# Kernel tuning notes

Measured on AMD Instinct MI355X. Metric: run time of the kernel, lower is better.

## Reference

```python
import jax, jax.numpy as jnp
import numpy as np

H = 1024      # hidden_dim
NH = 16       # num_heads
HD = H // NH  # head_dim
EPS = 1e-12
SCALE = float(np.sqrt(H))


def setup_inputs() -> dict:
    key = jax.random.key(0)
    ks = jax.random.split(key, 12)
    S, B = 2048, 2
    inp = {
        "query": jax.random.normal(ks[0], (S, B, 2 * H), jnp.float32),
        "key":   jax.random.normal(ks[1], (S, B, H), jnp.float32),
        "value": jax.random.normal(ks[2], (S, B, H), jnp.float32),
        # gating params (zeros in torch init, but randomize for a meaningful test)
        "qs": jax.random.normal(ks[3], (1, 1, H), jnp.float32) * 0.02,
        "ks_p": jax.random.normal(ks[4], (1, 1, H), jnp.float32) * 0.02,
        "vs": jax.random.normal(ks[5], (1, 1, H), jnp.float32) * 0.02,
        # Overparam vq: Linear(H, 2H)
        "vq_w": jax.random.normal(ks[6], (2 * H, H), jnp.float32) * (1.0 / np.sqrt(H)),
        "vq_b": jax.random.normal(ks[7], (2 * H,), jnp.float32) * 0.02,
        # q_linear: Linear(2H, H)
        "ql_w": jax.random.normal(ks[8], (H, 2 * H), jnp.float32) * (1.0 / np.sqrt(2 * H)),
        "ql_b": jax.random.normal(ks[9], (H,), jnp.float32) * 0.02,
        # LayerNorm(H)
        "ln_g": jnp.ones((H,), jnp.float32),
        "ln_b": jnp.zeros((H,), jnp.float32),
    }
    return inp


def _layernorm(x, g, b):
    mu = jnp.mean(x, axis=-1, keepdims=True)
    var = jnp.mean(jnp.square(x - mu), axis=-1, keepdims=True)
    return (x - mu) * jax.lax.rsqrt(var + EPS) * g + b


def reference(query, key, value, qs, ks_p, vs, vq_w, vq_b, ql_w, ql_b, ln_g, ln_b):
    # gate vectors
    qsig = jax.nn.sigmoid(qs)            # [1,1,H]
    ksig = jax.nn.sigmoid(ks_p)          # [1,1,H]
    # vq = Overparam(sigmoid(vs)): c,f = l1(x).split(H); sigmoid(f)*tanh(c)
    h = jax.nn.sigmoid(vs) @ vq_w.T + vq_b   # [1,1,2H]
    c, f = h[..., :H], h[..., H:]
    vsig = jax.nn.sigmoid(f) * jnp.tanh(c)   # [1,1,H]

    q = qsig * _layernorm(query @ ql_w.T + ql_b, ln_g, ln_b)  # [S,B,H]
    k = ksig * key
    v = vsig * value

    # batch-first
    q = jnp.transpose(q, (1, 0, 2))  # [B,Q,H]
    k = jnp.transpose(k, (1, 0, 2))  # [B,K,H]
    v = jnp.transpose(v, (1, 0, 2))
    B, Q, _ = q.shape
    K = k.shape[1]

    qh = q.reshape(B, Q, NH, HD)
    kh = k.reshape(B, K, NH, HD)
    vh = v.reshape(B, K, NH, HD)

    scores = jnp.einsum('bqhd,bkhd->bhqk', qh, kh) / SCALE
    w = jax.nn.softmax(scores, axis=-1)                # [B,NH,Q,K]
    out = jnp.einsum('bhqk,bkhd->bqhd', w, vh).reshape(B, Q, H)
    # torch code's final .transpose(0,1) is not assigned -> output is [Q,B,H]
    return jnp.transpose(out, (1, 0, 2))
```

## Files before the change

kernel.cpp:

```cpp
#include <hip/hip_runtime.h>

typedef __bf16 bf16x8 __attribute__((ext_vector_type(8)));
typedef float f32x4 __attribute__((ext_vector_type(4)));
typedef unsigned short u16x8 __attribute__((ext_vector_type(8)));
typedef unsigned short u16x4 __attribute__((ext_vector_type(4)));
typedef unsigned short u16;
typedef unsigned int u32;


#define LOG2E 1.4426950408889634f

__device__ __forceinline__ float b2f(u16 u) {
  union { unsigned int i; float f; } x; x.i = ((unsigned int)u) << 16; return x.f;
}
__device__ __forceinline__ u16 f2b(float f) {
  union { float f; unsigned int i; } x; x.f = f;
  unsigned int r = (x.i + 0x7fffu + ((x.i >> 16) & 1u)) >> 16;
  return (u16)r;
}
__device__ __forceinline__ float sigm(float x) { return 1.0f / (1.0f + __expf(-x)); }
__device__ __forceinline__ u32 cvtpk(float lo, float hi) {
  u32 r; asm("v_cvt_pk_bf16_f32 %0, %1, %2" : "=v"(r) : "v"(lo), "v"(hi)); return r;
}

__device__ __forceinline__ void async16(u16* lds, const u16* g) {
  __builtin_amdgcn_global_load_lds((const __attribute__((address_space(1))) void*)g,
                                   (__attribute__((address_space(3))) void*)lds, 16, 0, 0);
}

__global__ __launch_bounds__(256) void k_cvt_h(const float4* __restrict__ q, u16x4* __restrict__ qd,
                                               const float4* __restrict__ w, u16x4* __restrict__ wd,
                                               const float4* __restrict__ k, u16x4* __restrict__ kd,
                                               const float4* __restrict__ v, u16x4* __restrict__ vd,
                                               const float* __restrict__ vs,
                                               const float* __restrict__ vq_w,
                                               const float* __restrict__ vq_b,
                                               float* __restrict__ h,
                                               const float* __restrict__ qs,
                                               const float* __restrict__ ks,
                                               float* __restrict__ gate) {
  __shared__ float svs[1024];
  int b = blockIdx.x;
  int t = threadIdx.x;
  if (b < 2048) {
#pragma unroll
    for (int vb = b; vb < 18432; vb += 2048) {
      const float4* s; u16x4* d; int i;
      if (vb < 8192)       { s = q; d = qd; i = vb * 256 + t; }
      else if (vb < 10240) { s = w; d = wd; i = (vb - 8192) * 256 + t; }
      else if (vb < 14336) { s = k; d = kd; i = (vb - 10240) * 256 + t; }
      else                 { s = v; d = vd; i = (vb - 14336) * 256 + t; }
      float4 x = s[i];
      u16x4 o; o[0] = f2b(x.x); o[1] = f2b(x.y); o[2] = f2b(x.z); o[3] = f2b(x.w);
      d[i] = o;
    }
    return;
  }
  if (b < 2560) {
    for (int i = t; i < 1024; i += 256) svs[i] = sigm(vs[i]);
    __syncthreads();
    int wave = t >> 6, lane = t & 63;
    int row = (b - 2048) * 4 + wave;
    const float4* w4 = (const float4*)(vq_w + (size_t)row * 1024);
    const float4* s4 = (const float4*)svs;
    float acc = 0.f;
#pragma unroll
    for (int kk = 0; kk < 4; ++kk) {
      float4 wv = w4[kk * 64 + lane];
      float4 sv = s4[kk * 64 + lane];
      acc += wv.x * sv.x + wv.y * sv.y + wv.z * sv.z + wv.w * sv.w;
    }
#pragma unroll
    for (int off = 1; off < 64; off <<= 1) acc += __shfl_xor(acc, off);
    if (lane == 0) h[row] = acc + vq_b[row];
    return;
  }
  int ch = (b - 2560) * 256 + t;
  gate[ch] = sigm(qs[ch]) * sigm(ks[ch]) * (LOG2E / 32.0f);
}

__global__ __launch_bounds__(256) void k_gemm(const u16* __restrict__ A,
                                              const u16* __restrict__ Bt,
                                              u16* __restrict__ C) {
  __shared__ __align__(16) u16 As[2][64 * 32];
  __shared__ __align__(16) u16 Bs[2][128 * 32];
  int tid = threadIdx.x;
  int wave = tid >> 6, lane = tid & 63;
  int l15 = lane & 15, quad = lane >> 4;
  int bx = blockIdx.x & 511;
  int kh = blockIdx.x >> 9;
  int kofs = kh << 10;
  int m0 = (bx >> 3) * 64;
  int n0 = (bx & 7) * 128;
  int wm = (wave >> 1) * 32, wn = (wave & 1) * 64;
  f32x4 acc[2][4] = {};
  int c1 = tid, c2 = tid + 256;
  const u16* gaA = A + (size_t)(m0 + (c1 >> 2)) * 2048 + kofs + (c1 & 3) * 8;
  const u16* gb1 = Bt + (size_t)(n0 + (c1 >> 2)) * 2048 + kofs + (c1 & 3) * 8;
  const u16* gb2 = Bt + (size_t)(n0 + (c2 >> 2)) * 2048 + kofs + (c2 & 3) * 8;
  int lofs = wave * 512;
  async16(As[0] + lofs, gaA);
  async16(Bs[0] + lofs, gb1); async16(Bs[0] + 2048 + lofs, gb2);
  gaA += 32; gb1 += 32; gb2 += 32;
  __syncthreads();
  for (int kt = 0; kt < 32; ++kt) {
    int cur = kt & 1;
    if (kt < 31) {
      async16(As[cur ^ 1] + lofs, gaA);
      async16(Bs[cur ^ 1] + lofs, gb1); async16(Bs[cur ^ 1] + 2048 + lofs, gb2);
      gaA += 32; gb1 += 32; gb2 += 32;
    }
    bf16x8 af[2], bfr[4];
#pragma unroll
    for (int mt = 0; mt < 2; ++mt)
      af[mt] = *(const bf16x8*)(As[cur] + (wm + mt * 16 + l15) * 32 + quad * 8);
#pragma unroll
    for (int nt = 0; nt < 4; ++nt)
      bfr[nt] = *(const bf16x8*)(Bs[cur] + (wn + nt * 16 + l15) * 32 + quad * 8);
#pragma unroll
    for (int mt = 0; mt < 2; ++mt)
#pragma unroll
      for (int nt = 0; nt < 4; ++nt)
        acc[mt][nt] = __builtin_amdgcn_mfma_f32_16x16x32_bf16(af[mt], bfr[nt], acc[mt][nt], 0, 0, 0);
    __syncthreads();
  }
  u16* Cp = C + (size_t)kh * 4096 * 1024;
#pragma unroll
  for (int mt = 0; mt < 2; ++mt) {
#pragma unroll
    for (int r = 0; r < 4; ++r) {
      int m = m0 + wm + mt * 16 + quad * 4 + r;
      u16* crow = Cp + (size_t)m * 1024 + n0 + wn + l15;
#pragma unroll
      for (int nt = 0; nt < 4; ++nt) crow[nt * 16] = f2b(acc[mt][nt][r]);
    }
  }
}

__global__ __launch_bounds__(256) void k_ln(const u16* __restrict__ qpre0,
                                            const u16* __restrict__ qpre1,
                                            const float* __restrict__ ql_b,
                                            const float* __restrict__ ln_g,
                                            const float* __restrict__ ln_b,
                                            const float* __restrict__ gate,
                                            u16* __restrict__ qatt) {
  int t = threadIdx.x;
  int wave = t >> 6, lane = t & 63;
  int row = blockIdx.x * 4 + wave;
  int ch0 = lane * 16;
  const u16* p0 = qpre0 + (size_t)row * 1024 + ch0;
  const u16* p1 = qpre1 + (size_t)row * 1024 + ch0;
  u16x8 a0 = *(const u16x8*)p0;
  u16x8 a1 = *(const u16x8*)(p0 + 8);
  u16x8 c0 = *(const u16x8*)p1;
  u16x8 c1 = *(const u16x8*)(p1 + 8);
  float qb[16];
#pragma unroll
  for (int i = 0; i < 4; ++i) *(float4*)&qb[i * 4] = *(const float4*)(ql_b + ch0 + i * 4);
  float v[16];
  float s = 0.f, ss = 0.f;
#pragma unroll
  for (int j = 0; j < 8; ++j) {
    v[j] = b2f(a0[j]) + b2f(c0[j]) + qb[j];
    v[8 + j] = b2f(a1[j]) + b2f(c1[j]) + qb[8 + j];
  }
#pragma unroll
  for (int j = 0; j < 16; ++j) { s += v[j]; ss += v[j] * v[j]; }
#pragma unroll
  for (int off = 1; off < 64; off <<= 1) { s += __shfl_xor(s, off); ss += __shfl_xor(ss, off); }
  float mu = s * (1.f / 1024.f);
  float rstd = rsqrtf(ss * (1.f / 1024.f) - mu * mu + 1e-12f);
  float g_[16], bb[16], gt[16];
#pragma unroll
  for (int i = 0; i < 4; ++i) {
    *(float4*)&g_[i * 4] = *(const float4*)(ln_g + ch0 + i * 4);
    *(float4*)&bb[i * 4] = *(const float4*)(ln_b + ch0 + i * 4);
    *(float4*)&gt[i * 4] = *(const float4*)(gate + ch0 + i * 4);
  }
  int sidx = row >> 1, b = row & 1;
  int hh = ch0 >> 6, hd0 = ch0 & 63;
  u16* dst = qatt + ((size_t)(b * 16 + hh) * 2048 + sidx) * 64 + hd0;
  u16x8 o0, o1;
#pragma unroll
  for (int j = 0; j < 8; ++j) {
    o0[j] = f2b(((v[j] - mu) * rstd * g_[j] + bb[j]) * gt[j]);
    o1[j] = f2b(((v[8 + j] - mu) * rstd * g_[8 + j] + bb[8 + j]) * gt[8 + j]);
  }
  *(u16x8*)dst = o0;
  *(u16x8*)(dst + 8) = o1;
}

__device__ __forceinline__ f32x4 mfma16(bf16x8 a, bf16x8 b, f32x4 c) {
  return __builtin_amdgcn_mfma_f32_16x16x32_bf16(a, b, c, 0, 0, 0);
}

template <int CUR>
__device__ __forceinline__ void attn_iter(bool pref,
                                          const bf16x8 (&qf)[4][2],
                                          const u16*& kp, const u16*& vp,
                                          u16 (&Ks)[2][64 * 64], u16 (&Vt)[2][64 * 64],
                                          f32x4 (&oacc)[4][4], float (&l_i)[4],
                                          int kdst, int chbase, int pcol,
                                          int l15, int kh, int kcolA, int kcolB, int vcol) {
  const u16* kt0 = Ks[CUR] + (kh * 32 + l15) * 64;
  bf16x8 kA0 = *(const bf16x8*)(kt0 + kcolA);
  bf16x8 kB0 = *(const bf16x8*)(kt0 + kcolB);
  bf16x8 kA1 = *(const bf16x8*)(kt0 + 16 * 64 + kcolA);
  bf16x8 kB1 = *(const bf16x8*)(kt0 + 16 * 64 + kcolB);
  f32x4 sacc[4][2] = {};
  __builtin_amdgcn_s_setprio(1);
#pragma unroll
  for (int f = 0; f < 4; ++f) {
    sacc[f][0] = mfma16(kA0, qf[f][0], sacc[f][0]);
    sacc[f][0] = mfma16(kB0, qf[f][1], sacc[f][0]);
    sacc[f][1] = mfma16(kA1, qf[f][0], sacc[f][1]);
    sacc[f][1] = mfma16(kB1, qf[f][1], sacc[f][1]);
  }
  __builtin_amdgcn_s_setprio(0);
  u16x8 kr0, kr1, va, vq;
  if (pref) {
    kp += 64 * 2048;
    kr0 = *(const u16x8*)kp;
    kr1 = *(const u16x8*)(kp + (size_t)32 * 2048);
    vp += 64 * 2048;
    va = *(const u16x8*)vp;
    vq = *(const u16x8*)(vp + 2048);
  }
  union U8 { u32 w[4]; bf16x8 v; };
  bf16x8 pa[4];
#pragma unroll
  for (int f = 0; f < 4; ++f) {
    float pe[2][4];
#pragma unroll
    for (int kn = 0; kn < 2; ++kn)
#pragma unroll
      for (int r = 0; r < 4; ++r) pe[kn][r] = __builtin_amdgcn_exp2f(sacc[f][kn][r]);
    l_i[f] += (pe[0][0] + pe[0][1] + pe[0][2] + pe[0][3]) +
              (pe[1][0] + pe[1][1] + pe[1][2] + pe[1][3]);
    U8 t;
    t.w[0] = cvtpk(pe[0][0], pe[0][1]); t.w[1] = cvtpk(pe[0][2], pe[0][3]);
    t.w[2] = cvtpk(pe[1][0], pe[1][1]); t.w[3] = cvtpk(pe[1][2], pe[1][3]);
    pa[f] = t.v;
  }
  const u16* vt0 = Vt[CUR];
  __builtin_amdgcn_s_setprio(1);
#pragma unroll
  for (int nt = 0; nt < 4; ++nt) {
    bf16x8 vF = *(const bf16x8*)(vt0 + (nt * 16 + l15) * 64 + vcol);
    oacc[0][nt] = mfma16(pa[0], vF, oacc[0][nt]);
    oacc[1][nt] = mfma16(pa[1], vF, oacc[1][nt]);
    oacc[2][nt] = mfma16(pa[2], vF, oacc[2][nt]);
    oacc[3][nt] = mfma16(pa[3], vF, oacc[3][nt]);
  }
  __builtin_amdgcn_s_setprio(0);
  if (pref) {
    u16* kd = (u16*)Ks[CUR ^ 1];
    *(u16x8*)(kd + kdst) = kr0;
    *(u16x8*)(kd + kdst + 2048) = kr1;
    u16* vd = (u16*)Vt[CUR ^ 1];
#pragma unroll
    for (int c = 0; c < 8; ++c) {
      u32 pk2 = (u32)va[c] | ((u32)vq[c] << 16);
      *(u32*)&vd[(chbase + c) * 64 + (pcol ^ (c << 3))] = pk2;
    }
  }
  __syncthreads();
}

__device__ __forceinline__ void donate2(float* Rw, float* Lxp,
                                        const f32x4 (&o0)[4], const f32x4 (&o1)[4],
                                        float l0, float l1, int quad, int l15) {
#pragma unroll
  for (int nt = 0; nt < 4; ++nt)
#pragma unroll
    for (int r = 0; r < 4; ++r) {
      Rw[(quad * 4 + r) * 64 + nt * 16 + l15] = o0[nt][r];
      Rw[(16 + quad * 4 + r) * 64 + nt * 16 + l15] = o1[nt][r];
    }
  if (quad == 0) { Lxp[l15] = l0; Lxp[16 + l15] = l1; }
}

__device__ __forceinline__ void epi2(const float* Rr, const float* Lxp,
                                     const f32x4 (&o0)[4], const f32x4 (&o1)[4],
                                     float l0, float l1, const float (&vsg)[4],
                                     float* __restrict__ out, int sqbase, int b, int h,
                                     int quad, int l15) {
#pragma unroll
  for (int ff = 0; ff < 2; ++ff) {
    float lt = (ff == 0 ? l0 : l1) + Lxp[ff * 16 + l15];
#pragma unroll
    for (int r = 0; r < 4; ++r) {
      int sq = sqbase + ff * 16 + quad * 4 + r;
      float inv = 1.0f / __shfl(lt, quad * 4 + r);
      float* orow = out + ((size_t)sq * 2 + b) * 1024 + h * 64;
#pragma unroll
      for (int nt = 0; nt < 4; ++nt) {
        float own = (ff == 0 ? o0[nt][r] : o1[nt][r]);
        orow[nt * 16 + l15] =
            (own + Rr[(ff * 16 + quad * 4 + r) * 64 + nt * 16 + l15]) * inv * vsg[nt];
      }
    }
  }
}

__global__ __launch_bounds__(256, 2) void k_attn(const u16* __restrict__ qatt,
                                                 const u16* __restrict__ key,
                                                 const u16* __restrict__ value,
                                                 const float* __restrict__ hbuf,
                                                 float* __restrict__ out) {
  int bh = blockIdx.x & 31;
  int qt = blockIdx.x >> 5;
  int b = bh >> 4, h = bh & 15;
  int tid = threadIdx.x, wave = tid >> 6, lane = tid & 63;
  int l15 = lane & 15, quad = lane >> 4;
  int qh = wave >> 1, kh = wave & 1;
  int q0 = qt * 128;

  __shared__ __align__(16) u16 Ks[2][64 * 64];
  __shared__ __align__(16) u16 Vt[2][64 * 64];
  __shared__ float Lx[2][2][32];

  bf16x8 qf[4][2];
#pragma unroll
  for (int f = 0; f < 4; ++f) {
    const u16* qrow = qatt + ((size_t)bh * 2048 + q0 + qh * 64 + f * 16 + l15) * 64 + quad * 8;
    qf[f][0] = *(const bf16x8*)qrow;
    qf[f][1] = *(const bf16x8*)(qrow + 32);
  }

  const u16* kb = key + (size_t)b * 1024 + (size_t)h * 64;
  const u16* vb = value + (size_t)b * 1024 + (size_t)h * 64;

  int krow = tid >> 3;
  int kchk = (tid & 7) * 8;
  const u16* kp = kb + (size_t)krow * 2048 + kchk;
  int kdst = krow * 64 + (kchk ^ ((krow & 7) << 3));

  int p = lane & 31;
  int chbase = wave * 16 + (lane >> 5) * 8;
  const u16* vp = vb + (size_t)2 * p * 2048 + chbase;
  int kk = 2 * p;
  int pcol = ((kk >> 5) & 1) * 32 + ((kk >> 2) & 3) * 8 + ((kk >> 4) & 1) * 4 + (kk & 3);
  int swr = (l15 & 7) << 3;
  int kcolA = (8 * quad) ^ swr;
  int kcolB = (32 + 8 * quad) ^ swr;
  int vcol = (kh * 32 + 8 * quad) ^ swr;

  {
    u16x8 kr0 = *(const u16x8*)kp;
    u16x8 kr1 = *(const u16x8*)(kp + (size_t)32 * 2048);
    *(u16x8*)(&Ks[0][kdst]) = kr0;
    *(u16x8*)(&Ks[0][kdst + 2048]) = kr1;
    u16x8 va = *(const u16x8*)vp;
    u16x8 vq = *(const u16x8*)(vp + 2048);
#pragma unroll
    for (int c = 0; c < 8; ++c) {
      u32 pk2 = (u32)va[c] | ((u32)vq[c] << 16);
      *(u32*)&Vt[0][(chbase + c) * 64 + (pcol ^ (c << 3))] = pk2;
    }
  }
  __syncthreads();

  f32x4 oacc[4][4] = {};
  float l_i[4] = {};

  for (int kt = 0; kt < 32; kt += 2) {
    attn_iter<0>(true, qf, kp, vp, Ks, Vt, oacc, l_i, kdst, chbase, pcol, l15, kh, kcolA, kcolB, vcol);
    attn_iter<1>(kt < 30, qf, kp, vp, Ks, Vt, oacc, l_i, kdst, chbase, pcol, l15, kh, kcolA, kcolB, vcol);
  }

#pragma unroll
  for (int f = 0; f < 4; ++f) {
    float l = l_i[f];
    l += __shfl_xor(l, 16);
    l += __shfl_xor(l, 32);
    l_i[f] = l;
  }
  float* base = (qh == 0) ? (float*)&Ks[0][0] : (float*)&Vt[0][0];
  if (kh == 0) {
    donate2(base + 2048, &Lx[qh][1][0], oacc[2], oacc[3], l_i[2], l_i[3], quad, l15);
  } else {
    donate2(base, &Lx[qh][0][0], oacc[0], oacc[1], l_i[0], l_i[1], quad, l15);
  }
  __syncthreads();
  float vsg[4];
#pragma unroll
  for (int nt = 0; nt < 4; ++nt) {
    int ch = h * 64 + nt * 16 + l15;
    vsg[nt] = sigm(hbuf[1024 + ch]) * tanhf(hbuf[ch]);
  }
  int sqbase = q0 + qh * 64 + kh * 32;
  if (kh == 0) {
    epi2(base, &Lx[qh][0][0], oacc[0], oacc[1], l_i[0], l_i[1], vsg, out, sqbase, b, h, quad, l15);
  } else {
    epi2(base + 2048, &Lx[qh][1][0], oacc[2], oacc[3], l_i[2], l_i[3], vsg, out, sqbase, b, h, quad, l15);
  }
}

extern "C" void kernel_launch(void* const* d_in, const int* in_sizes, int n_in,
                              void* d_out, int out_size, void* d_ws, size_t ws_size,
                              hipStream_t stream) {
  (void)in_sizes; (void)n_in; (void)out_size; (void)ws_size;
  const float* query = (const float*)d_in[0];
  const float* key   = (const float*)d_in[1];
  const float* value = (const float*)d_in[2];
  const float* qs    = (const float*)d_in[3];
  const float* ksp   = (const float*)d_in[4];
  const float* vs    = (const float*)d_in[5];
  const float* vq_w  = (const float*)d_in[6];
  const float* vq_b  = (const float*)d_in[7];
  const float* ql_w  = (const float*)d_in[8];
  const float* ql_b  = (const float*)d_in[9];
  const float* ln_g  = (const float*)d_in[10];
  const float* ln_b  = (const float*)d_in[11];
  float* out = (float*)d_out;

  float* ws = (float*)d_ws;
  float* h    = ws;
  float* gate = ws + 2048;
  u16* qpre  = (u16*)(ws + 4096);
  u16* qbf   = qpre + (size_t)2 * 4096 * 1024;
  u16* qatt  = qbf;
  u16* wbf   = qbf + (size_t)4096 * 2048;
  u16* kbf   = wbf + (size_t)1024 * 2048;
  u16* vbf   = kbf + (size_t)4096 * 1024;

  hipLaunchKernelGGL(k_cvt_h, dim3(2564), dim3(256), 0, stream,
                     (const float4*)query, (u16x4*)qbf,
                     (const float4*)ql_w,  (u16x4*)wbf,
                     (const float4*)key,   (u16x4*)kbf,
                     (const float4*)value, (u16x4*)vbf,
                     vs, vq_w, vq_b, h, qs, ksp, gate);
  hipLaunchKernelGGL(k_gemm, dim3(1024), dim3(256), 0, stream, qbf, wbf, qpre);
  hipLaunchKernelGGL(k_ln,   dim3(1024), dim3(256), 0, stream, qpre, qpre + (size_t)4096 * 1024,
                     ql_b, ln_g, ln_b, gate, qatt);
  hipLaunchKernelGGL(k_attn, dim3(512),  dim3(256), 0, stream, qatt, kbf, vbf, h, out);
}
```

Before: 218.5 us.

## Fuse all four stages into one persistent kernel with grid barriers

Replaces the four separate launches (convert, GEMM, layernorm, attention) with a single 512-block persistent kernel that runs each stage in sequence, separated by atomic-counter grid barriers. A memset before the launch clears the barrier counters. The goal is to remove launch overhead and the gaps between kernels. In exchange, the earlier stages lose parallelism (the conversion and GEMM now use 512 blocks instead of 2564 and 1024), every stage waits on a spin barrier, and correctness depends on all 512 blocks being resident at once.

```diff
diff --git a/kernel.cpp b/kernel.cpp
--- a/kernel.cpp
+++ b/kernel.cpp
@@ -9,6 +9,7 @@
 
 
 #define LOG2E 1.4426950408889634f
+#define NBLK 512u
 
 __device__ __forceinline__ float b2f(u16 u) {
   union { unsigned int i; float f; } x; x.i = ((unsigned int)u) << 16; return x.f;
@@ -22,73 +23,33 @@
 __device__ __forceinline__ u32 cvtpk(float lo, float hi) {
   u32 r; asm("v_cvt_pk_bf16_f32 %0, %1, %2" : "=v"(r) : "v"(lo), "v"(hi)); return r;
 }
-
 __device__ __forceinline__ void async16(u16* lds, const u16* g) {
   __builtin_amdgcn_global_load_lds((const __attribute__((address_space(1))) void*)g,
                                    (__attribute__((address_space(3))) void*)lds, 16, 0, 0);
 }
-
-__global__ __launch_bounds__(256) void k_cvt_h(const float4* __restrict__ q, u16x4* __restrict__ qd,
-                                               const float4* __restrict__ w, u16x4* __restrict__ wd,
-                                               const float4* __restrict__ k, u16x4* __restrict__ kd,
-                                               const float4* __restrict__ v, u16x4* __restrict__ vd,
-                                               const float* __restrict__ vs,
-                                               const float* __restrict__ vq_w,
-                                               const float* __restrict__ vq_b,
-                                               float* __restrict__ h,
-                                               const float* __restrict__ qs,
-                                               const float* __restrict__ ks,
-                                               float* __restrict__ gate) {
-  __shared__ float svs[1024];
-  int b = blockIdx.x;
-  int t = threadIdx.x;
-  if (b < 2048) {
-#pragma unroll
-    for (int vb = b; vb < 18432; vb += 2048) {
-      const float4* s; u16x4* d; int i;
-      if (vb < 8192)       { s = q; d = qd; i = vb * 256 + t; }
-      else if (vb < 10240) { s = w; d = wd; i = (vb - 8192) * 256 + t; }
-      else if (vb < 14336) { s = k; d = kd; i = (vb - 10240) * 256 + t; }
-      else                 { s = v; d = vd; i = (vb - 14336) * 256 + t; }
-      float4 x = s[i];
-      u16x4 o; o[0] = f2b(x.x); o[1] = f2b(x.y); o[2] = f2b(x.z); o[3] = f2b(x.w);
-      d[i] = o;
-    }
-    return;
-  }
-  if (b < 2560) {
-    for (int i = t; i < 1024; i += 256) svs[i] = sigm(vs[i]);
-    __syncthreads();
-    int wave = t >> 6, lane = t & 63;
-    int row = (b - 2048) * 4 + wave;
-    const float4* w4 = (const float4*)(vq_w + (size_t)row * 1024);
-    const float4* s4 = (const float4*)svs;
-    float acc = 0.f;
-#pragma unroll
-    for (int kk = 0; kk < 4; ++kk) {
-      float4 wv = w4[kk * 64 + lane];
-      float4 sv = s4[kk * 64 + lane];
-      acc += wv.x * sv.x + wv.y * sv.y + wv.z * sv.z + wv.w * sv.w;
-    }
-#pragma unroll
-    for (int off = 1; off < 64; off <<= 1) acc += __shfl_xor(acc, off);
-    if (lane == 0) h[row] = acc + vq_b[row];
-    return;
-  }
-  int ch = (b - 2560) * 256 + t;
-  gate[ch] = sigm(qs[ch]) * sigm(ks[ch]) * (LOG2E / 32.0f);
-}
-
-__global__ __launch_bounds__(256) void k_gemm(const u16* __restrict__ A,
-                                              const u16* __restrict__ Bt,
-                                              u16* __restrict__ C) {
-  __shared__ __align__(16) u16 As[2][64 * 32];
-  __shared__ __align__(16) u16 Bs[2][128 * 32];
-  int tid = threadIdx.x;
+__device__ __forceinline__ f32x4 mfma16(bf16x8 a, bf16x8 b, f32x4 c) {
+  return __builtin_amdgcn_mfma_f32_16x16x32_bf16(a, b, c, 0, 0, 0);
+}
+
+__device__ __forceinline__ void gbar(unsigned* c) {
+  __syncthreads();
+  if (threadIdx.x == 0) {
+    __threadfence();
+    __hip_atomic_fetch_add(c, 1u, __ATOMIC_ACQ_REL, __HIP_MEMORY_SCOPE_AGENT);
+    while (__hip_atomic_load(c, __ATOMIC_ACQUIRE, __HIP_MEMORY_SCOPE_AGENT) < NBLK)
+      __builtin_amdgcn_s_sleep(2);
+    __threadfence();
+  }
+  __syncthreads();
+}
+
+__device__ __forceinline__ void gemm_tile(int bid, const u16* __restrict__ A,
+                                          const u16* __restrict__ Bt, u16* __restrict__ C,
+                                          u16* As, u16* Bs, int tid) {
   int wave = tid >> 6, lane = tid & 63;
   int l15 = lane & 15, quad = lane >> 4;
-  int bx = blockIdx.x & 511;
-  int kh = blockIdx.x >> 9;
+  int bx = bid & 511;
+  int kh = bid >> 9;
   int kofs = kh << 10;
   int m0 = (bx >> 3) * 64;
   int n0 = (bx & 7) * 128;
@@ -99,29 +60,30 @@
   const u16* gb1 = Bt + (size_t)(n0 + (c1 >> 2)) * 2048 + kofs + (c1 & 3) * 8;
   const u16* gb2 = Bt + (size_t)(n0 + (c2 >> 2)) * 2048 + kofs + (c2 & 3) * 8;
   int lofs = wave * 512;
-  async16(As[0] + lofs, gaA);
-  async16(Bs[0] + lofs, gb1); async16(Bs[0] + 2048 + lofs, gb2);
+  async16(As + lofs, gaA);
+  async16(Bs + lofs, gb1); async16(Bs + 2048 + lofs, gb2);
   gaA += 32; gb1 += 32; gb2 += 32;
   __syncthreads();
   for (int kt = 0; kt < 32; ++kt) {
     int cur = kt & 1;
     if (kt < 31) {
-      async16(As[cur ^ 1] + lofs, gaA);
-      async16(Bs[cur ^ 1] + lofs, gb1); async16(Bs[cur ^ 1] + 2048 + lofs, gb2);
+      async16(As + (cur ^ 1) * 2048 + lofs, gaA);
+      async16(Bs + (cur ^ 1) * 4096 + lofs, gb1);
+      async16(Bs + (cur ^ 1) * 4096 + 2048 + lofs, gb2);
       gaA += 32; gb1 += 32; gb2 += 32;
     }
     bf16x8 af[2], bfr[4];
 #pragma unroll
     for (int mt = 0; mt < 2; ++mt)
-      af[mt] = *(const bf16x8*)(As[cur] + (wm + mt * 16 + l15) * 32 + quad * 8);
+      af[mt] = *(const bf16x8*)(As + cur * 2048 + (wm + mt * 16 + l15) * 32 + quad * 8);
 #pragma unroll
     for (int nt = 0; nt < 4; ++nt)
-      bfr[nt] = *(const bf16x8*)(Bs[cur] + (wn + nt * 16 + l15) * 32 + quad * 8);
+      bfr[nt] = *(const bf16x8*)(Bs + cur * 4096 + (wn + nt * 16 + l15) * 32 + quad * 8);
 #pragma unroll
     for (int mt = 0; mt < 2; ++mt)
 #pragma unroll
       for (int nt = 0; nt < 4; ++nt)
-        acc[mt][nt] = __builtin_amdgcn_mfma_f32_16x16x32_bf16(af[mt], bfr[nt], acc[mt][nt], 0, 0, 0);
+        acc[mt][nt] = mfma16(af[mt], bfr[nt], acc[mt][nt]);
     __syncthreads();
   }
   u16* Cp = C + (size_t)kh * 4096 * 1024;
@@ -135,74 +97,17 @@
       for (int nt = 0; nt < 4; ++nt) crow[nt * 16] = f2b(acc[mt][nt][r]);
     }
   }
-}
-
-__global__ __launch_bounds__(256) void k_ln(const u16* __restrict__ qpre0,
-                                            const u16* __restrict__ qpre1,
-                                            const float* __restrict__ ql_b,
-                                            const float* __restrict__ ln_g,
-                                            const float* __restrict__ ln_b,
-                                            const float* __restrict__ gate,
-                                            u16* __restrict__ qatt) {
-  int t = threadIdx.x;
-  int wave = t >> 6, lane = t & 63;
-  int row = blockIdx.x * 4 + wave;
-  int ch0 = lane * 16;
-  const u16* p0 = qpre0 + (size_t)row * 1024 + ch0;
-  const u16* p1 = qpre1 + (size_t)row * 1024 + ch0;
-  u16x8 a0 = *(const u16x8*)p0;
-  u16x8 a1 = *(const u16x8*)(p0 + 8);
-  u16x8 c0 = *(const u16x8*)p1;
-  u16x8 c1 = *(const u16x8*)(p1 + 8);
-  float qb[16];
-#pragma unroll
-  for (int i = 0; i < 4; ++i) *(float4*)&qb[i * 4] = *(const float4*)(ql_b + ch0 + i * 4);
-  float v[16];
-  float s = 0.f, ss = 0.f;
-#pragma unroll
-  for (int j = 0; j < 8; ++j) {
-    v[j] = b2f(a0[j]) + b2f(c0[j]) + qb[j];
-    v[8 + j] = b2f(a1[j]) + b2f(c1[j]) + qb[8 + j];
-  }
-#pragma unroll
-  for (int j = 0; j < 16; ++j) { s += v[j]; ss += v[j] * v[j]; }
-#pragma unroll
-  for (int off = 1; off < 64; off <<= 1) { s += __shfl_xor(s, off); ss += __shfl_xor(ss, off); }
-  float mu = s * (1.f / 1024.f);
-  float rstd = rsqrtf(ss * (1.f / 1024.f) - mu * mu + 1e-12f);
-  float g_[16], bb[16], gt[16];
-#pragma unroll
-  for (int i = 0; i < 4; ++i) {
-    *(float4*)&g_[i * 4] = *(const float4*)(ln_g + ch0 + i * 4);
-    *(float4*)&bb[i * 4] = *(const float4*)(ln_b + ch0 + i * 4);
-    *(float4*)&gt[i * 4] = *(const float4*)(gate + ch0 + i * 4);
-  }
-  int sidx = row >> 1, b = row & 1;
-  int hh = ch0 >> 6, hd0 = ch0 & 63;
-  u16* dst = qatt + ((size_t)(b * 16 + hh) * 2048 + sidx) * 64 + hd0;
-  u16x8 o0, o1;
-#pragma unroll
-  for (int j = 0; j < 8; ++j) {
-    o0[j] = f2b(((v[j] - mu) * rstd * g_[j] + bb[j]) * gt[j]);
-    o1[j] = f2b(((v[8 + j] - mu) * rstd * g_[8 + j] + bb[8 + j]) * gt[8 + j]);
-  }
-  *(u16x8*)dst = o0;
-  *(u16x8*)(dst + 8) = o1;
-}
-
-__device__ __forceinline__ f32x4 mfma16(bf16x8 a, bf16x8 b, f32x4 c) {
-  return __builtin_amdgcn_mfma_f32_16x16x32_bf16(a, b, c, 0, 0, 0);
 }
 
 template <int CUR>
 __device__ __forceinline__ void attn_iter(bool pref,
                                           const bf16x8 (&qf)[4][2],
                                           const u16*& kp, const u16*& vp,
-                                          u16 (&Ks)[2][64 * 64], u16 (&Vt)[2][64 * 64],
+                                          u16* KsB, u16* VtB,
                                           f32x4 (&oacc)[4][4], float (&l_i)[4],
                                           int kdst, int chbase, int pcol,
                                           int l15, int kh, int kcolA, int kcolB, int vcol) {
-  const u16* kt0 = Ks[CUR] + (kh * 32 + l15) * 64;
+  const u16* kt0 = KsB + CUR * 4096 + (kh * 32 + l15) * 64;
   bf16x8 kA0 = *(const bf16x8*)(kt0 + kcolA);
   bf16x8 kB0 = *(const bf16x8*)(kt0 + kcolB);
   bf16x8 kA1 = *(const bf16x8*)(kt0 + 16 * 64 + kcolA);
@@ -242,7 +147,7 @@
     t.w[2] = cvtpk(pe[1][0], pe[1][1]); t.w[3] = cvtpk(pe[1][2], pe[1][3]);
     pa[f] = t.v;
   }
-  const u16* vt0 = Vt[CUR];
+  const u16* vt0 = VtB + CUR * 4096;
   __builtin_amdgcn_s_setprio(1);
 #pragma unroll
   for (int nt = 0; nt < 4; ++nt) {
@@ -254,10 +159,10 @@
   }
   __builtin_amdgcn_s_setprio(0);
   if (pref) {
-    u16* kd = (u16*)Ks[CUR ^ 1];
+    u16* kd = KsB + (CUR ^ 1) * 4096;
     *(u16x8*)(kd + kdst) = kr0;
     *(u16x8*)(kd + kdst + 2048) = kr1;
-    u16* vd = (u16*)Vt[CUR ^ 1];
+    u16* vd = VtB + (CUR ^ 1) * 4096;
 #pragma unroll
     for (int c = 0; c < 8; ++c) {
       u32 pk2 = (u32)va[c] | ((u32)vq[c] << 16);
@@ -303,97 +208,214 @@
   }
 }
 
-__global__ __launch_bounds__(256, 2) void k_attn(const u16* __restrict__ qatt,
-                                                 const u16* __restrict__ key,
-                                                 const u16* __restrict__ value,
-                                                 const float* __restrict__ hbuf,
-                                                 float* __restrict__ out) {
-  int bh = blockIdx.x & 31;
-  int qt = blockIdx.x >> 5;
-  int b = bh >> 4, h = bh & 15;
+__global__ __launch_bounds__(256, 2) void k_all(const float* __restrict__ query,
+                                                const float* __restrict__ key_,
+                                                const float* __restrict__ value,
+                                                const float* __restrict__ qs,
+                                                const float* __restrict__ ksp,
+                                                const float* __restrict__ vs,
+                                                const float* __restrict__ vq_w,
+                                                const float* __restrict__ vq_b,
+                                                const float* __restrict__ ql_w,
+                                                const float* __restrict__ ql_b,
+                                                const float* __restrict__ ln_g,
+                                                const float* __restrict__ ln_b,
+                                                float* __restrict__ out,
+                                                float* __restrict__ ws) {
+  __shared__ __align__(16) u16 SMEM[16640];
+  int blk = blockIdx.x;
   int tid = threadIdx.x, wave = tid >> 6, lane = tid & 63;
-  int l15 = lane & 15, quad = lane >> 4;
-  int qh = wave >> 1, kh = wave & 1;
-  int q0 = qt * 128;
-
-  __shared__ __align__(16) u16 Ks[2][64 * 64];
-  __shared__ __align__(16) u16 Vt[2][64 * 64];
-  __shared__ float Lx[2][2][32];
-
-  bf16x8 qf[4][2];
-#pragma unroll
-  for (int f = 0; f < 4; ++f) {
-    const u16* qrow = qatt + ((size_t)bh * 2048 + q0 + qh * 64 + f * 16 + l15) * 64 + quad * 8;
-    qf[f][0] = *(const bf16x8*)qrow;
-    qf[f][1] = *(const bf16x8*)(qrow + 32);
-  }
-
-  const u16* kb = key + (size_t)b * 1024 + (size_t)h * 64;
-  const u16* vb = value + (size_t)b * 1024 + (size_t)h * 64;
-
-  int krow = tid >> 3;
-  int kchk = (tid & 7) * 8;
-  const u16* kp = kb + (size_t)krow * 2048 + kchk;
-  int kdst = krow * 64 + (kchk ^ ((krow & 7) << 3));
-
-  int p = lane & 31;
-  int chbase = wave * 16 + (lane >> 5) * 8;
-  const u16* vp = vb + (size_t)2 * p * 2048 + chbase;
-  int kk = 2 * p;
-  int pcol = ((kk >> 5) & 1) * 32 + ((kk >> 2) & 3) * 8 + ((kk >> 4) & 1) * 4 + (kk & 3);
-  int swr = (l15 & 7) << 3;
-  int kcolA = (8 * quad) ^ swr;
-  int kcolB = (32 + 8 * quad) ^ swr;
-  int vcol = (kh * 32 + 8 * quad) ^ swr;
+
+  float* h    = ws;
+  float* gate = ws + 2048;
+  unsigned* bar = (unsigned*)(ws + 3072);
+  u16* qpre  = (u16*)(ws + 4096);
+  u16* qbf   = qpre + (size_t)2 * 4096 * 1024;
+  u16* qatt  = qbf;
+  u16* wbf   = qbf + (size_t)4096 * 2048;
+  u16* kbf   = wbf + (size_t)1024 * 2048;
+  u16* vbf   = kbf + (size_t)4096 * 1024;
 
   {
-    u16x8 kr0 = *(const u16x8*)kp;
-    u16x8 kr1 = *(const u16x8*)(kp + (size_t)32 * 2048);
-    *(u16x8*)(&Ks[0][kdst]) = kr0;
-    *(u16x8*)(&Ks[0][kdst + 2048]) = kr1;
-    u16x8 va = *(const u16x8*)vp;
-    u16x8 vq = *(const u16x8*)(vp + 2048);
-#pragma unroll
-    for (int c = 0; c < 8; ++c) {
-      u32 pk2 = (u32)va[c] | ((u32)vq[c] << 16);
-      *(u32*)&Vt[0][(chbase + c) * 64 + (pcol ^ (c << 3))] = pk2;
-    }
-  }
-  __syncthreads();
-
-  f32x4 oacc[4][4] = {};
-  float l_i[4] = {};
-
-  for (int kt = 0; kt < 32; kt += 2) {
-    attn_iter<0>(true, qf, kp, vp, Ks, Vt, oacc, l_i, kdst, chbase, pcol, l15, kh, kcolA, kcolB, vcol);
-    attn_iter<1>(kt < 30, qf, kp, vp, Ks, Vt, oacc, l_i, kdst, chbase, pcol, l15, kh, kcolA, kcolB, vcol);
-  }
-
-#pragma unroll
-  for (int f = 0; f < 4; ++f) {
-    float l = l_i[f];
-    l += __shfl_xor(l, 16);
-    l += __shfl_xor(l, 32);
-    l_i[f] = l;
-  }
-  float* base = (qh == 0) ? (float*)&Ks[0][0] : (float*)&Vt[0][0];
-  if (kh == 0) {
-    donate2(base + 2048, &Lx[qh][1][0], oacc[2], oacc[3], l_i[2], l_i[3], quad, l15);
-  } else {
-    donate2(base, &Lx[qh][0][0], oacc[0], oacc[1], l_i[0], l_i[1], quad, l15);
-  }
-  __syncthreads();
-  float vsg[4];
-#pragma unroll
-  for (int nt = 0; nt < 4; ++nt) {
-    int ch = h * 64 + nt * 16 + l15;
-    vsg[nt] = sigm(hbuf[1024 + ch]) * tanhf(hbuf[ch]);
-  }
-  int sqbase = q0 + qh * 64 + kh * 32;
-  if (kh == 0) {
-    epi2(base, &Lx[qh][0][0], oacc[0], oacc[1], l_i[0], l_i[1], vsg, out, sqbase, b, h, quad, l15);
-  } else {
-    epi2(base + 2048, &Lx[qh][1][0], oacc[2], oacc[3], l_i[2], l_i[3], vsg, out, sqbase, b, h, quad, l15);
+    const float4* q4 = (const float4*)query;
+    const float4* w4 = (const float4*)ql_w;
+    const float4* k4 = (const float4*)key_;
+    const float4* v4 = (const float4*)value;
+    for (int vb = blk; vb < 18432; vb += 512) {
+      const float4* s; u16x4* d; int i;
+      if (vb < 8192)       { s = q4; d = (u16x4*)qbf; i = vb * 256 + tid; }
+      else if (vb < 10240) { s = w4; d = (u16x4*)wbf; i = (vb - 8192) * 256 + tid; }
+      else if (vb < 14336) { s = k4; d = (u16x4*)kbf; i = (vb - 10240) * 256 + tid; }
+      else                 { s = v4; d = (u16x4*)vbf; i = (vb - 14336) * 256 + tid; }
+      float4 x = s[i];
+      u16x4 o; o[0] = f2b(x.x); o[1] = f2b(x.y); o[2] = f2b(x.z); o[3] = f2b(x.w);
+      d[i] = o;
+    }
+    float* svs = (float*)SMEM;
+    for (int i = tid; i < 1024; i += 256) svs[i] = sigm(vs[i]);
+    __syncthreads();
+    int row = blk * 4 + wave;
+    const float4* wv4 = (const float4*)(vq_w + (size_t)row * 1024);
+    const float4* s4 = (const float4*)svs;
+    float acc = 0.f;
+#pragma unroll
+    for (int kk = 0; kk < 4; ++kk) {
+      float4 wv = wv4[kk * 64 + lane];
+      float4 sv = s4[kk * 64 + lane];
+      acc += wv.x * sv.x + wv.y * sv.y + wv.z * sv.z + wv.w * sv.w;
+    }
+#pragma unroll
+    for (int off = 1; off < 64; off <<= 1) acc += __shfl_xor(acc, off);
+    if (lane == 0) h[row] = acc + vq_b[row];
+    if (tid < 2) {
+      int ch = blk * 2 + tid;
+      gate[ch] = sigm(qs[ch]) * sigm(ksp[ch]) * (LOG2E / 32.0f);
+    }
+  }
+  gbar(bar + 0);
+
+  {
+    u16* As = SMEM;
+    u16* Bs = SMEM + 4096;
+    gemm_tile(blk, qbf, wbf, qpre, As, Bs, tid);
+    gemm_tile(blk + 512, qbf, wbf, qpre, As, Bs, tid);
+  }
+  gbar(bar + 1);
+
+  {
+    const u16* qpre1 = qpre + (size_t)4096 * 1024;
+    int ch0 = lane * 16;
+    float qb[16], g_[16], bb[16], gt[16];
+#pragma unroll
+    for (int i = 0; i < 4; ++i) {
+      *(float4*)&qb[i * 4] = *(const float4*)(ql_b + ch0 + i * 4);
+      *(float4*)&g_[i * 4] = *(const float4*)(ln_g + ch0 + i * 4);
+      *(float4*)&bb[i * 4] = *(const float4*)(ln_b + ch0 + i * 4);
+      *(float4*)&gt[i * 4] = *(const float4*)(gate + ch0 + i * 4);
+    }
+#pragma unroll
+    for (int rr = 0; rr < 2; ++rr) {
+      int row = blk * 8 + rr * 4 + wave;
+      const u16* p0 = qpre + (size_t)row * 1024 + ch0;
+      const u16* p1 = qpre1 + (size_t)row * 1024 + ch0;
+      u16x8 a0 = *(const u16x8*)p0;
+      u16x8 a1 = *(const u16x8*)(p0 + 8);
+      u16x8 c0 = *(const u16x8*)p1;
+      u16x8 c1 = *(const u16x8*)(p1 + 8);
+      float v[16];
+      float s = 0.f, ss = 0.f;
+#pragma unroll
+      for (int j = 0; j < 8; ++j) {
+        v[j] = b2f(a0[j]) + b2f(c0[j]) + qb[j];
+        v[8 + j] = b2f(a1[j]) + b2f(c1[j]) + qb[8 + j];
+      }
+#pragma unroll
+      for (int j = 0; j < 16; ++j) { s += v[j]; ss += v[j] * v[j]; }
+#pragma unroll
+      for (int off = 1; off < 64; off <<= 1) { s += __shfl_xor(s, off); ss += __shfl_xor(ss, off); }
+      float mu = s * (1.f / 1024.f);
+      float rstd = rsqrtf(ss * (1.f / 1024.f) - mu * mu + 1e-12f);
+      int sidx = row >> 1, b = row & 1;
+      int hh = ch0 >> 6, hd0 = ch0 & 63;
+      u16* dst = qatt + ((size_t)(b * 16 + hh) * 2048 + sidx) * 64 + hd0;
+      u16x8 o0, o1;
+#pragma unroll
+      for (int j = 0; j < 8; ++j) {
+        o0[j] = f2b(((v[j] - mu) * rstd * g_[j] + bb[j]) * gt[j]);
+        o1[j] = f2b(((v[8 + j] - mu) * rstd * g_[8 + j] + bb[8 + j]) * gt[8 + j]);
+      }
+      *(u16x8*)dst = o0;
+      *(u16x8*)(dst + 8) = o1;
+    }
+  }
+  gbar(bar + 2);
+
+  {
+    u16* Ks = SMEM;
+    u16* Vt = SMEM + 8192;
+    float* Lx = (float*)(SMEM + 16384);
+    int bh = blk & 31;
+    int qt = blk >> 5;
+    int b = bh >> 4, hd = bh & 15;
+    int l15 = lane & 15, quad = lane >> 4;
+    int qh = wave >> 1, kh = wave & 1;
+    int q0 = qt * 128;
+
+    bf16x8 qf[4][2];
+#pragma unroll
+    for (int f = 0; f < 4; ++f) {
+      const u16* qrow = qatt + ((size_t)bh * 2048 + q0 + qh * 64 + f * 16 + l15) * 64 + quad * 8;
+      qf[f][0] = *(const bf16x8*)qrow;
+      qf[f][1] = *(const bf16x8*)(qrow + 32);
+    }
+
+    const u16* kb = kbf + (size_t)b * 1024 + (size_t)hd * 64;
+    const u16* vb = vbf + (size_t)b * 1024 + (size_t)hd * 64;
+
+    int krow = tid >> 3;
+    int kchk = (tid & 7) * 8;
+    const u16* kp = kb + (size_t)krow * 2048 + kchk;
+    int kdst = krow * 64 + (kchk ^ ((krow & 7) << 3));
+
+    int p = lane & 31;
+    int chbase = wave * 16 + (lane >> 5) * 8;
+    const u16* vp = vb + (size_t)2 * p * 2048 + chbase;
+    int kk = 2 * p;
+    int pcol = ((kk >> 5) & 1) * 32 + ((kk >> 2) & 3) * 8 + ((kk >> 4) & 1) * 4 + (kk & 3);
+    int swr = (l15 & 7) << 3;
+    int kcolA = (8 * quad) ^ swr;
+    int kcolB = (32 + 8 * quad) ^ swr;
+    int vcol = (kh * 32 + 8 * quad) ^ swr;
+
+    {
+      u16x8 kr0 = *(const u16x8*)kp;
+      u16x8 kr1 = *(const u16x8*)(kp + (size_t)32 * 2048);
+      *(u16x8*)(Ks + kdst) = kr0;
+      *(u16x8*)(Ks + kdst + 2048) = kr1;
+      u16x8 va = *(const u16x8*)vp;
+      u16x8 vq = *(const u16x8*)(vp + 2048);
+#pragma unroll
+      for (int c = 0; c < 8; ++c) {
+        u32 pk2 = (u32)va[c] | ((u32)vq[c] << 16);
+        *(u32*)&Vt[(chbase + c) * 64 + (pcol ^ (c << 3))] = pk2;
+      }
+    }
+    __syncthreads();
+
+    f32x4 oacc[4][4] = {};
+    float l_i[4] = {};
+
+    for (int kt = 0; kt < 32; kt += 2) {
+      attn_iter<0>(true, qf, kp, vp, Ks, Vt, oacc, l_i, kdst, chbase, pcol, l15, kh, kcolA, kcolB, vcol);
+      attn_iter<1>(kt < 30, qf, kp, vp, Ks, Vt, oacc, l_i, kdst, chbase, pcol, l15, kh, kcolA, kcolB, vcol);
+    }
+
+#pragma unroll
+    for (int f = 0; f < 4; ++f) {
+      float l = l_i[f];
+      l += __shfl_xor(l, 16);
+      l += __shfl_xor(l, 32);
+      l_i[f] = l;
+    }
+    float* base = (qh == 0) ? (float*)Ks : (float*)Vt;
+    if (kh == 0) {
+      donate2(base + 2048, Lx + (qh * 2 + 1) * 32, oacc[2], oacc[3], l_i[2], l_i[3], quad, l15);
+    } else {
+      donate2(base, Lx + (qh * 2 + 0) * 32, oacc[0], oacc[1], l_i[0], l_i[1], quad, l15);
+    }
+    __syncthreads();
+    float vsg[4];
+#pragma unroll
+    for (int nt = 0; nt < 4; ++nt) {
+      int ch = hd * 64 + nt * 16 + l15;
+      vsg[nt] = sigm(h[1024 + ch]) * tanhf(h[ch]);
+    }
+    int sqbase = q0 + qh * 64 + kh * 32;
+    if (kh == 0) {
+      epi2(base, Lx + (qh * 2 + 0) * 32, oacc[0], oacc[1], l_i[0], l_i[1], vsg, out, sqbase, b, hd, quad, l15);
+    } else {
+      epi2(base + 2048, Lx + (qh * 2 + 1) * 32, oacc[2], oacc[3], l_i[2], l_i[3], vsg, out, sqbase, b, hd, quad, l15);
+    }
   }
 }
 
@@ -414,25 +436,10 @@
   const float* ln_g  = (const float*)d_in[10];
   const float* ln_b  = (const float*)d_in[11];
   float* out = (float*)d_out;
-
   float* ws = (float*)d_ws;
-  float* h    = ws;
-  float* gate = ws + 2048;
-  u16* qpre  = (u16*)(ws + 4096);
-  u16* qbf   = qpre + (size_t)2 * 4096 * 1024;
-  u16* qatt  = qbf;
-  u16* wbf   = qbf + (size_t)4096 * 2048;
-  u16* kbf   = wbf + (size_t)1024 * 2048;
-  u16* vbf   = kbf + (size_t)4096 * 1024;
-
-  hipLaunchKernelGGL(k_cvt_h, dim3(2564), dim3(256), 0, stream,
-                     (const float4*)query, (u16x4*)qbf,
-                     (const float4*)ql_w,  (u16x4*)wbf,
-                     (const float4*)key,   (u16x4*)kbf,
-                     (const float4*)value, (u16x4*)vbf,
-                     vs, vq_w, vq_b, h, qs, ksp, gate);
-  hipLaunchKernelGGL(k_gemm, dim3(1024), dim3(256), 0, stream, qbf, wbf, qpre);
-  hipLaunchKernelGGL(k_ln,   dim3(1024), dim3(256), 0, stream, qpre, qpre + (size_t)4096 * 1024,
-                     ql_b, ln_g, ln_b, gate, qatt);
-  hipLaunchKernelGGL(k_attn, dim3(512),  dim3(256), 0, stream, qatt, kbf, vbf, h, out);
-}
+
+  hipMemsetAsync((char*)d_ws + 3072 * sizeof(float), 0, 64, stream);
+  hipLaunchKernelGGL(k_all, dim3(512), dim3(256), 0, stream,
+                     query, key, value, qs, ksp, vs, vq_w, vq_b, ql_w, ql_b,
+                     ln_g, ln_b, out, ws);
+}
```

Measured after the change: 470.8 us. +115.5%, slower.
